# Optimization experiments

Measured on AMD Instinct MI355X. Metric: run time of the kernel, lower is better.

Reference implementation:

```python
import jax, jax.numpy as jnp
import numpy as np

N = 4096
IN_DIM, HID, OUT_DIM = 512, 256, 64
PROP_STEP = 10
LAM_HAT = 0.9
SCAD_A = 3.7
EPS = 1e-8


def setup_inputs() -> dict:
    key = jax.random.key(0)
    kA, kF, k1, k2 = jax.random.split(key, 4)
    # sparse symmetric 0/1 adjacency, zero diagonal (add_loops adds I later)
    u = jax.random.uniform(kA, (N, N), dtype=jnp.float32)
    A = (u < 0.005).astype(jnp.float32)
    A = jnp.maximum(A, A.T)
    A = A * (1.0 - jnp.eye(N, dtype=jnp.float32))
    F = jax.random.normal(kF, (N, IN_DIM), dtype=jnp.float32)
    W1 = jax.random.normal(k1, (IN_DIM, HID), dtype=jnp.float32) / np.sqrt(IN_DIM)
    b1 = jnp.zeros((HID,), dtype=jnp.float32)
    W2 = jax.random.normal(k2, (HID, OUT_DIM), dtype=jnp.float32) / np.sqrt(HID)
    b2 = jnp.zeros((OUT_DIM,), dtype=jnp.float32)
    raw_gamma = jnp.zeros((PROP_STEP,), dtype=jnp.float32)
    return {"A": A, "F": F, "W1": W1, "b1": b1, "W2": W2, "b2": b2,
            "raw_gamma": raw_gamma}


def reference(A, F, W1, b1, W2, b2, raw_gamma):
    lam = 1.0 / LAM_HAT - 1.0
    a = SCAD_A
    # MLP (dropout inactive at inference)
    F0 = jax.nn.relu(F @ W1 + b1) @ W2 + b2            # [N, out_dim]
    eye = jnp.eye(A.shape[0], dtype=A.dtype)
    A = A + eye                                        # add_loops
    D = A.sum(-1)                                      # [N]
    D_sq = jnp.sqrt(D)[:, None]                        # [N, 1]
    A_tilde = A / D_sq / D_sq.T                        # sym_norm: D^-1/2 A D^-1/2
    gammas = jax.nn.sigmoid(raw_gamma) * 2.0           # per-layer gamma in (0, 2)

    def step(Fc, gamma_k):
        Fn = Fc / D_sq
        nrm = jnp.linalg.norm(Fn, axis=-1, keepdims=True)
        Fu = Fn / jnp.maximum(nrm, 1e-12)
        # cosine distance in [0, 2]; detached as in torch (.detach())
        y = jax.lax.stop_gradient(1.0 - Fu @ Fu.T)     # [N, N]
        lam_k = jnp.maximum(gamma_k / a, EPS)
        t = a * lam_k
        safe_y = jnp.where(y <= 0.0, 1.0, y)
        w_mid = (t - y) / ((a - 1.0) * safe_y)
        # SCAD weight: 1 for y<=lam_k, linear decay on [lam_k, a*lam_k], 0 beyond
        W = jnp.where(y <= lam_k, 1.0, jnp.where(y <= t, w_mid, 0.0))
        W = W * (1.0 - eye)
        W = jnp.where(jnp.isnan(W), 1.0, W)
        Q_hat = ((W * A).sum(-1) / D + lam)[:, None]   # [N, 1]
        F_new = (W * A_tilde) @ Fc / Q_hat + lam * F0 / Q_hat
        return F_new, None

    F_out, _ = jax.lax.scan(step, F0, gammas)
    return F_out
```

## Files before the change

### kernel.cpp

```cpp
#include <hip/hip_runtime.h>
#include <hip/hip_bf16.h>

#define N_NODES 4096
#define IN_DIM  512
#define HID_DIM 256
#define OUT_DIM 64
#define PROP_STEP 10
#define MAX_DEG 128
#define GEMM_BLOCKS 512
#define SCAN_BLOCKS 512
#define LAM_CONST (1.0f/0.9f - 1.0f)
#define SCAD_A 3.7f

__device__ __forceinline__ ushort f2bf(float f) {
    unsigned u = __float_as_uint(f);
    unsigned r = (u + 0x7FFFu + ((u >> 16) & 1u)) >> 16;
    return (ushort)r;
}
__device__ __forceinline__ unsigned pack2(float lo, float hi) {
    return (unsigned)f2bf(lo) | ((unsigned)f2bf(hi) << 16);
}
__device__ __forceinline__ float bflo(unsigned u) { return __uint_as_float(u << 16); }
__device__ __forceinline__ float bfhi(unsigned u) { return __uint_as_float(u & 0xFFFF0000u); }
__device__ __forceinline__ float4 f4add(float4 a, float4 b) {
    return make_float4(a.x + b.x, a.y + b.y, a.z + b.z, a.w + b.w);
}

#define FMA32(A0, A1, WV) \
    ac0.x = fmaf(A0.x, WV.x, ac0.x); ac0.y = fmaf(A0.x, WV.y, ac0.y); \
    ac0.z = fmaf(A0.x, WV.z, ac0.z); ac0.w = fmaf(A0.x, WV.w, ac0.w); \
    ac1.x = fmaf(A0.y, WV.x, ac1.x); ac1.y = fmaf(A0.y, WV.y, ac1.y); \
    ac1.z = fmaf(A0.y, WV.z, ac1.z); ac1.w = fmaf(A0.y, WV.w, ac1.w); \
    ac2.x = fmaf(A0.z, WV.x, ac2.x); ac2.y = fmaf(A0.z, WV.y, ac2.y); \
    ac2.z = fmaf(A0.z, WV.z, ac2.z); ac2.w = fmaf(A0.z, WV.w, ac2.w); \
    ac3.x = fmaf(A0.w, WV.x, ac3.x); ac3.y = fmaf(A0.w, WV.y, ac3.y); \
    ac3.z = fmaf(A0.w, WV.z, ac3.z); ac3.w = fmaf(A0.w, WV.w, ac3.w); \
    ac4.x = fmaf(A1.x, WV.x, ac4.x); ac4.y = fmaf(A1.x, WV.y, ac4.y); \
    ac4.z = fmaf(A1.x, WV.z, ac4.z); ac4.w = fmaf(A1.x, WV.w, ac4.w); \
    ac5.x = fmaf(A1.y, WV.x, ac5.x); ac5.y = fmaf(A1.y, WV.y, ac5.y); \
    ac5.z = fmaf(A1.y, WV.z, ac5.z); ac5.w = fmaf(A1.y, WV.w, ac5.w); \
    ac6.x = fmaf(A1.z, WV.x, ac6.x); ac6.y = fmaf(A1.z, WV.y, ac6.y); \
    ac6.z = fmaf(A1.z, WV.z, ac6.z); ac6.w = fmaf(A1.z, WV.w, ac6.w); \
    ac7.x = fmaf(A1.w, WV.x, ac7.x); ac7.y = fmaf(A1.w, WV.y, ac7.y); \
    ac7.z = fmaf(A1.w, WV.z, ac7.z); ac7.w = fmaf(A1.w, WV.w, ac7.w);

#define CONS(KK, WV) { \
    float4 a0_ = *(const float4*)&sF[(KK) * 8];     \
    float4 a1_ = *(const float4*)&sF[(KK) * 8 + 4]; \
    FMA32(a0_, a1_, WV) }

#define P2ROW(HV, PV) \
    PV.x = fmaf(HV.x, w0.x, PV.x); PV.y = fmaf(HV.x, w0.y, PV.y); \
    PV.z = fmaf(HV.x, w0.z, PV.z); PV.w = fmaf(HV.x, w0.w, PV.w); \
    PV.x = fmaf(HV.y, w1.x, PV.x); PV.y = fmaf(HV.y, w1.y, PV.y); \
    PV.z = fmaf(HV.y, w1.z, PV.z); PV.w = fmaf(HV.y, w1.w, PV.w); \
    PV.x = fmaf(HV.z, w2.x, PV.x); PV.y = fmaf(HV.z, w2.y, PV.y); \
    PV.z = fmaf(HV.z, w2.z, PV.z); PV.w = fmaf(HV.z, w2.w, PV.w); \
    PV.x = fmaf(HV.w, w3.x, PV.x); PV.y = fmaf(HV.w, w3.y, PV.y); \
    PV.z = fmaf(HV.w, w3.z, PV.z); PV.w = fmaf(HV.w, w3.w, PV.w);

__global__ __launch_bounds__(256, 4) void build_all(
    const float* __restrict__ A, const float* __restrict__ F,
    const float* __restrict__ W1, const float* __restrict__ b1,
    const float* __restrict__ W2, const float* __restrict__ b2,
    float* __restrict__ F0,
    int* __restrict__ ell, int* __restrict__ deg,
    float* __restrict__ invD, float* __restrict__ invDsq)
{
    __shared__ float smem[8192];
    if (blockIdx.x >= SCAN_BLOCKS) {
        float* sF = smem;
        int t    = threadIdx.x;
        int lane = t & 63, wid = t >> 6;
        int m0   = (blockIdx.x - SCAN_BLOCKS) * 8;
        {
            int r = t & 7, kc = (t >> 3) * 16;
            const float* src = F + (size_t)(m0 + r) * IN_DIM + kc;
#pragma unroll
            for (int j = 0; j < 4; j++) {
                float4 v = *(const float4*)(src + j * 4);
                sF[(kc + j * 4 + 0) * 8 + r] = v.x;
                sF[(kc + j * 4 + 1) * 8 + r] = v.y;
                sF[(kc + j * 4 + 2) * 8 + r] = v.z;
                sF[(kc + j * 4 + 3) * 8 + r] = v.w;
            }
        }
        __syncthreads();
        int cg = lane;
        int kw = wid * 128;
        const float* Wp = W1 + (size_t)kw * HID_DIM + cg * 4;
        float4 ac0 = {0,0,0,0}, ac1 = {0,0,0,0}, ac2 = {0,0,0,0}, ac3 = {0,0,0,0};
        float4 ac4 = {0,0,0,0}, ac5 = {0,0,0,0}, ac6 = {0,0,0,0}, ac7 = {0,0,0,0};
        float4 wa0 = *(const float4*)(Wp + 0 * HID_DIM);
        float4 wa1 = *(const float4*)(Wp + 1 * HID_DIM);
        float4 wa2 = *(const float4*)(Wp + 2 * HID_DIM);
        float4 wa3 = *(const float4*)(Wp + 3 * HID_DIM);
        float4 wb0 = *(const float4*)(Wp + 4 * HID_DIM);
        float4 wb1 = *(const float4*)(Wp + 5 * HID_DIM);
        float4 wb2 = *(const float4*)(Wp + 6 * HID_DIM);
        float4 wb3 = *(const float4*)(Wp + 7 * HID_DIM);
        for (int kb = 0; kb < 128; kb += 8) {
            int k0 = kw + kb;
            CONS(k0 + 0, wa0) CONS(k0 + 1, wa1) CONS(k0 + 2, wa2) CONS(k0 + 3, wa3)
            if (kb + 8 < 128) {
                const float* wn = Wp + (size_t)(kb + 8) * HID_DIM;
                wa0 = *(const float4*)(wn);
                wa1 = *(const float4*)(wn + HID_DIM);
                wa2 = *(const float4*)(wn + 2 * HID_DIM);
                wa3 = *(const float4*)(wn + 3 * HID_DIM);
            }
            CONS(k0 + 4, wb0) CONS(k0 + 5, wb1) CONS(k0 + 6, wb2) CONS(k0 + 7, wb3)
            if (kb + 8 < 128) {
                const float* wn = Wp + (size_t)(kb + 12) * HID_DIM;
                wb0 = *(const float4*)(wn);
                wb1 = *(const float4*)(wn + HID_DIM);
                wb2 = *(const float4*)(wn + 2 * HID_DIM);
                wb3 = *(const float4*)(wn + 3 * HID_DIM);
            }
        }
        __syncthreads();
        {
            float* pp = smem + (size_t)wid * 2048;
            *(float4*)&pp[0 * 256 + cg * 4] = ac0;
            *(float4*)&pp[1 * 256 + cg * 4] = ac1;
            *(float4*)&pp[2 * 256 + cg * 4] = ac2;
            *(float4*)&pp[3 * 256 + cg * 4] = ac3;
            *(float4*)&pp[4 * 256 + cg * 4] = ac4;
            *(float4*)&pp[5 * 256 + cg * 4] = ac5;
            *(float4*)&pp[6 * 256 + cg * 4] = ac6;
            *(float4*)&pp[7 * 256 + cg * 4] = ac7;
        }
        __syncthreads();
        for (int i = t; i < 2048; i += 256) {
            float h = smem[i] + smem[i + 2048] + smem[i + 4096] + smem[i + 6144]
                    + b1[i & 255];
            smem[i] = fmaxf(h, 0.0f);
        }
        __syncthreads();
        float* sH = smem;
        int rgrp = lane >> 4;
        int cg2  = lane & 15;
        float4 p0 = {0,0,0,0}, p1 = {0,0,0,0};
        int kbase = wid * 64;
        for (int kq = 0; kq < 64; kq += 4) {
            int kg = kbase + kq;
            float4 h0 = *(const float4*)&sH[(rgrp * 2 + 0) * 256 + kg];
            float4 h1 = *(const float4*)&sH[(rgrp * 2 + 1) * 256 + kg];
            float4 w0 = *(const float4*)(W2 + (size_t)(kg + 0) * OUT_DIM + cg2 * 4);
            float4 w1 = *(const float4*)(W2 + (size_t)(kg + 1) * OUT_DIM + cg2 * 4);
            float4 w2 = *(const float4*)(W2 + (size_t)(kg + 2) * OUT_DIM + cg2 * 4);
            float4 w3 = *(const float4*)(W2 + (size_t)(kg + 3) * OUT_DIM + cg2 * 4);
            P2ROW(h0, p0) P2ROW(h1, p1)
        }
        __syncthreads();
        if (wid) {
            float* dst = smem + 2048 + (size_t)(wid - 1) * 512 + lane * 8;
            *(float4*)(dst + 0) = p0;
            *(float4*)(dst + 4) = p1;
        }
        __syncthreads();
        if (wid == 0) {
#pragma unroll
            for (int w = 0; w < 3; w++) {
                const float* s = smem + 2048 + (size_t)w * 512 + lane * 8;
                p0 = f4add(p0, *(const float4*)(s + 0));
                p1 = f4add(p1, *(const float4*)(s + 4));
            }
            float4 b2v = *(const float4*)(b2 + cg2 * 4);
            float* o = F0 + (size_t)(m0 + rgrp * 2) * OUT_DIM + cg2 * 4;
            *(float4*)(o + 0 * OUT_DIM) = f4add(p0, b2v);
            *(float4*)(o + 1 * OUT_DIM) = f4add(p1, b2v);
        }
    } else {
        int sb   = blockIdx.x;
        int lane = threadIdx.x & 63;
        int wid  = threadIdx.x >> 6;
        int w    = sb * 4 + wid;
        for (int rr = 0; rr < 2; rr++) {
            int row = w * 2 + rr;
            const float* Arow = A + (size_t)row * N_NODES;
            float4 ch[16];
#pragma unroll
            for (int c = 0; c < 16; c++)
                ch[c] = *(const float4*)(Arow + c * 256 + lane * 4);
            int* rdst = ell + (size_t)row * MAX_DEG;
            unsigned cnt = 0;
#pragma unroll
            for (int c = 0; c < 16; c++) {
                float4 v = ch[c];
                int colbase = c * 256 + lane * 4;
#pragma unroll
                for (int q = 0; q < 4; q++) {
                    float vv = (q == 0) ? v.x : (q == 1) ? v.y : (q == 2) ? v.z : v.w;
                    bool nz = (vv != 0.0f);
                    unsigned long long m = __ballot(nz);
                    unsigned rank = __builtin_amdgcn_mbcnt_hi(
                        (unsigned)(m >> 32),
                        __builtin_amdgcn_mbcnt_lo((unsigned)m, 0u));
                    unsigned pos = cnt + rank;
                    if (nz && pos < MAX_DEG) rdst[pos] = colbase + q;
                    cnt += (unsigned)__popcll(m);
                }
            }
            int c  = (cnt > MAX_DEG) ? MAX_DEG : (int)cnt;
            int pad = (c + 15) & ~15;
            if (pad > MAX_DEG) pad = MAX_DEG;
            if (lane >= c && lane < pad) rdst[lane] = row;
            int l2 = lane + 64;
            if (l2 >= c && l2 < pad) rdst[l2] = row;
            if (lane == 0) {
                deg[row] = c;
                float d = (float)(cnt + 1);
                invD[row] = 1.0f / d;
                invDsq[row] = rsqrtf(d);
            }
        }
    }
}

__global__ __launch_bounds__(256, 4) void propagate_f0(
    const float* __restrict__ F0,
    const int* __restrict__ ell, const int* __restrict__ deg,
    const float* __restrict__ invD, const float* __restrict__ invDsq,
    const float* __restrict__ raw_gamma,
    unsigned* __restrict__ Pout, float* __restrict__ nrmOut)
{
    int lane = threadIdx.x & 63;
    int wid  = threadIdx.x >> 6;
    int r    = __builtin_amdgcn_readfirstlane(blockIdx.x * 4 + wid);
    int g    = lane >> 3;
    int sl   = lane & 7;
    const float inv_am1 = 1.0f / (SCAD_A - 1.0f);

    float gamma = 2.0f / (1.0f + expf(-raw_gamma[0]));
    float lam_k = fmaxf(gamma / SCAD_A, 1e-8f);
    float tt    = SCAD_A * lam_k;

    int dg = deg[r];
    int pad = (dg + 15) & ~15;
    int npair = pad >> 4;
    const int* nb = ell + (size_t)r * MAX_DEG;
    int ed0 = (lane < pad)      ? nb[lane]      : r;
    int ed1 = (64 + lane < pad) ? nb[64 + lane] : r;

    float iDs = invDsq[r];
    const float4* f04 = (const float4*)(F0 + (size_t)r * OUT_DIM + sl * 8);
    float4 fa = f04[0], fb = f04[1];
    float f0v[8] = { fa.x, fa.y, fa.z, fa.w, fb.x, fb.y, fb.z, fb.w };
    float ui[8];
    float ssr = 0.0f;
#pragma unroll
    for (int q = 0; q < 8; q++) { ui[q] = f0v[q] * iDs; ssr += ui[q] * ui[q]; }
    ssr += __shfl_xor(ssr, 1, 64);
    ssr += __shfl_xor(ssr, 2, 64);
    ssr += __shfl_xor(ssr, 4, 64);
    float inv_nr = 1.0f / fmaxf(sqrtf(ssr), 1e-12f);
#pragma unroll
    for (int q = 0; q < 8; q++) ui[q] *= inv_nr;

    float acc[8] = {};
    float qsum = 0.0f;
    for (int it = 0; it < npair; ++it) {
        int e0 = it * 16 + g, e1 = e0 + 8;
        int src = (it < 4) ? ed0 : ed1;
        int j0 = __shfl(src, e0 & 63, 64);
        int j1 = __shfl(src, e1 & 63, 64);
        const float4* p0 = (const float4*)(F0 + (size_t)j0 * OUT_DIM + sl * 8);
        const float4* p1 = (const float4*)(F0 + (size_t)j1 * OUT_DIM + sl * 8);
        float4 x0 = p0[0], x1 = p0[1];
        float4 y0 = p1[0], y1 = p1[1];
        float d0 = invDsq[j0], d1 = invDsq[j1];
        float v0[8] = { x0.x*d0, x0.y*d0, x0.z*d0, x0.w*d0, x1.x*d0, x1.y*d0, x1.z*d0, x1.w*d0 };
        float v1[8] = { y0.x*d1, y0.y*d1, y0.z*d1, y0.w*d1, y1.x*d1, y1.y*d1, y1.z*d1, y1.w*d1 };
        float pa = 0.f, pb = 0.f, s0 = 0.f, s1 = 0.f;
#pragma unroll
        for (int q = 0; q < 8; q++) {
            pa += ui[q] * v0[q]; s0 += v0[q] * v0[q];
            pb += ui[q] * v1[q]; s1 += v1[q] * v1[q];
        }
        pa += __shfl_xor(pa, 1, 64); pb += __shfl_xor(pb, 1, 64);
        s0 += __shfl_xor(s0, 1, 64); s1 += __shfl_xor(s1, 1, 64);
        pa += __shfl_xor(pa, 2, 64); pb += __shfl_xor(pb, 2, 64);
        s0 += __shfl_xor(s0, 2, 64); s1 += __shfl_xor(s1, 2, 64);
        pa += __shfl_xor(pa, 4, 64); pb += __shfl_xor(pb, 4, 64);
        s0 += __shfl_xor(s0, 4, 64); s1 += __shfl_xor(s1, 4, 64);
        float n0 = fmaxf(sqrtf(s0), 1e-12f);
        float n1 = fmaxf(sqrtf(s1), 1e-12f);
        float ya = 1.0f - pa / n0, yb = 1.0f - pb / n1;
        float wa = (ya <= lam_k) ? 1.0f : ((ya <= tt) ? (tt - ya) * inv_am1 / ya : 0.0f);
        float wb = (yb <= lam_k) ? 1.0f : ((yb <= tt) ? (tt - yb) * inv_am1 / yb : 0.0f);
        if (e0 >= dg) wa = 0.0f;
        if (e1 >= dg) wb = 0.0f;
        qsum += wa + wb;
#pragma unroll
        for (int q = 0; q < 8; q++) acc[q] += wa * v0[q] + wb * v1[q];
    }

#pragma unroll
    for (int off = 8; off <= 32; off <<= 1) {
#pragma unroll
        for (int q = 0; q < 8; q++) acc[q] += __shfl_xor(acc[q], off, 64);
        qsum += __shfl_xor(qsum, off, 64);
    }

    float Qh  = qsum * invD[r] + LAM_CONST;
    float rQh = 1.0f / Qh;
    float res[8], fn[8];
    float ssq = 0.0f;
#pragma unroll
    for (int q = 0; q < 8; q++) {
        res[q] = (acc[q] * iDs + LAM_CONST * f0v[q]) * rQh;
        fn[q]  = res[q] * iDs;
        ssq   += fn[q] * fn[q];
    }
    ssq += __shfl_xor(ssq, 1, 64);
    ssq += __shfl_xor(ssq, 2, 64);
    ssq += __shfl_xor(ssq, 4, 64);
    float nrm = fmaxf(sqrtf(ssq), 1e-12f);
    float inv_n = 1.0f / nrm;
    if (lane < 8) {
        uint4 fuPk;
        fuPk.x = pack2(fn[0] * inv_n, fn[1] * inv_n);
        fuPk.y = pack2(fn[2] * inv_n, fn[3] * inv_n);
        fuPk.z = pack2(fn[4] * inv_n, fn[5] * inv_n);
        fuPk.w = pack2(fn[6] * inv_n, fn[7] * inv_n);
        *(uint4*)(Pout + (size_t)r * 32 + sl * 4) = fuPk;
    }
    if (lane == 0) nrmOut[r] = nrm;
}

__global__ __launch_bounds__(256, 4) void propagate(
    const unsigned* __restrict__ Pin, const float* __restrict__ nrmIn,
    const float* __restrict__ F0,
    const int* __restrict__ ell, const int* __restrict__ deg,
    const float* __restrict__ invD, const float* __restrict__ invDsq,
    const float* __restrict__ raw_gamma, int step,
    unsigned* __restrict__ Pout, float* __restrict__ nrmOut,
    float* __restrict__ FcOut, int writeNext, int writeOut)
{
    int lane = threadIdx.x & 63;
    int wid  = threadIdx.x >> 6;
    int r    = __builtin_amdgcn_readfirstlane(blockIdx.x * 4 + wid);
    int g    = lane >> 3;
    int sl   = lane & 7;
    const float inv_am1 = 1.0f / (SCAD_A - 1.0f);

    float gamma = 2.0f / (1.0f + expf(-raw_gamma[step]));
    float lam_k = fmaxf(gamma / SCAD_A, 1e-8f);
    float tt    = SCAD_A * lam_k;

    int dg = deg[r];
    int pad = (dg + 15) & ~15;
    int npair = pad >> 4;
    const int* nb = ell + (size_t)r * MAX_DEG;
    int ed0 = (lane < pad)      ? nb[lane]      : r;
    int ed1 = (64 + lane < pad) ? nb[64 + lane] : r;

    uint4 up = *(const uint4*)(Pin + (size_t)r * 32 + sl * 4);
    float ui[8] = { bflo(up.x), bfhi(up.x), bflo(up.y), bfhi(up.y),
                    bflo(up.z), bfhi(up.z), bflo(up.w), bfhi(up.w) };

    float acc[8] = {};
    float qsum = 0.0f;

    auto eidx = [&](int it_, int& J0, int& J1) {
        int e0_ = it_ * 16 + g;
        int src = (it_ < 4) ? ed0 : ed1;
        J0 = __shfl(src, e0_ & 63, 64);
        J1 = __shfl(src, (e0_ + 8) & 63, 64);
    };
    auto body = [&](int it_, uint4 U0, uint4 U1, float NR0, float NR1) {
        float pa = ui[0] * bflo(U0.x) + ui[1] * bfhi(U0.x) + ui[2] * bflo(U0.y) + ui[3] * bfhi(U0.y)
                 + ui[4] * bflo(U0.z) + ui[5] * bfhi(U0.z) + ui[6] * bflo(U0.w) + ui[7] * bfhi(U0.w);
        float pb = ui[0] * bflo(U1.x) + ui[1] * bfhi(U1.x) + ui[2] * bflo(U1.y) + ui[3] * bfhi(U1.y)
                 + ui[4] * bflo(U1.z) + ui[5] * bfhi(U1.z) + ui[6] * bflo(U1.w) + ui[7] * bfhi(U1.w);
        pa += __shfl_xor(pa, 1, 64); pb += __shfl_xor(pb, 1, 64);
        pa += __shfl_xor(pa, 2, 64); pb += __shfl_xor(pb, 2, 64);
        pa += __shfl_xor(pa, 4, 64); pb += __shfl_xor(pb, 4, 64);
        float ya = 1.0f - pa, yb = 1.0f - pb;
        float wa = (ya <= lam_k) ? 1.0f : ((ya <= tt) ? (tt - ya) * inv_am1 / ya : 0.0f);
        float wb = (yb <= lam_k) ? 1.0f : ((yb <= tt) ? (tt - yb) * inv_am1 / yb : 0.0f);
        int e0_ = it_ * 16 + g;
        if (e0_ >= dg)     wa = 0.0f;
        if (e0_ + 8 >= dg) wb = 0.0f;
        qsum += wa + wb;
        float wsa = wa * NR0;
        float wsb = wb * NR1;
        acc[0] += wsa * bflo(U0.x) + wsb * bflo(U1.x);
        acc[1] += wsa * bfhi(U0.x) + wsb * bfhi(U1.x);
        acc[2] += wsa * bflo(U0.y) + wsb * bflo(U1.y);
        acc[3] += wsa * bfhi(U0.y) + wsb * bfhi(U1.y);
        acc[4] += wsa * bflo(U0.z) + wsb * bflo(U1.z);
        acc[5] += wsa * bfhi(U0.z) + wsb * bfhi(U1.z);
        acc[6] += wsa * bflo(U0.w) + wsb * bflo(U1.w);
        acc[7] += wsa * bfhi(U0.w) + wsb * bfhi(U1.w);
    };

    if (npair > 0) {
        uint4 uA0, uA1, uB0, uB1;
        float nA0, nA1, nB0, nB1;
        int j0, j1;
        eidx(0, j0, j1);
        uA0 = *(const uint4*)(Pin + (size_t)j0 * 32 + sl * 4);
        uA1 = *(const uint4*)(Pin + (size_t)j1 * 32 + sl * 4);
        nA0 = nrmIn[j0]; nA1 = nrmIn[j1];
        int it = 0;
        while (true) {
            if (it + 1 < npair) {
                eidx(it + 1, j0, j1);
                uB0 = *(const uint4*)(Pin + (size_t)j0 * 32 + sl * 4);
                uB1 = *(const uint4*)(Pin + (size_t)j1 * 32 + sl * 4);
                nB0 = nrmIn[j0]; nB1 = nrmIn[j1];
            }
            body(it, uA0, uA1, nA0, nA1);
            ++it; if (it >= npair) break;
            if (it + 1 < npair) {
                eidx(it + 1, j0, j1);
                uA0 = *(const uint4*)(Pin + (size_t)j0 * 32 + sl * 4);
                uA1 = *(const uint4*)(Pin + (size_t)j1 * 32 + sl * 4);
                nA0 = nrmIn[j0]; nA1 = nrmIn[j1];
            }
            body(it, uB0, uB1, nB0, nB1);
            ++it; if (it >= npair) break;
        }
    }

#pragma unroll
    for (int off = 8; off <= 32; off <<= 1) {
#pragma unroll
        for (int q = 0; q < 8; q++) acc[q] += __shfl_xor(acc[q], off, 64);
        qsum += __shfl_xor(qsum, off, 64);
    }

    float iDs = invDsq[r];
    float Qh  = qsum * invD[r] + LAM_CONST;
    float rQh = 1.0f / Qh;
    const float4* f04 = (const float4*)(F0 + (size_t)r * OUT_DIM + sl * 8);
    float4 f0a = f04[0], f0b = f04[1];
    float f0v[8] = { f0a.x, f0a.y, f0a.z, f0a.w, f0b.x, f0b.y, f0b.z, f0b.w };
    float res[8];
#pragma unroll
    for (int q = 0; q < 8; q++) res[q] = (acc[q] * iDs + LAM_CONST * f0v[q]) * rQh;

    if (writeOut && lane < 8) {
        float4* o4 = (float4*)(FcOut + (size_t)r * OUT_DIM + sl * 8);
        o4[0] = make_float4(res[0], res[1], res[2], res[3]);
        o4[1] = make_float4(res[4], res[5], res[6], res[7]);
    }
    if (writeNext) {
        float fn[8];
        float ssq = 0.0f;
#pragma unroll
        for (int q = 0; q < 8; q++) { fn[q] = res[q] * iDs; ssq += fn[q] * fn[q]; }
        ssq += __shfl_xor(ssq, 1, 64);
        ssq += __shfl_xor(ssq, 2, 64);
        ssq += __shfl_xor(ssq, 4, 64);
        float nrm = fmaxf(sqrtf(ssq), 1e-12f);
        float inv_n = 1.0f / nrm;
        if (lane < 8) {
            uint4 fuPk;
            fuPk.x = pack2(fn[0] * inv_n, fn[1] * inv_n);
            fuPk.y = pack2(fn[2] * inv_n, fn[3] * inv_n);
            fuPk.z = pack2(fn[4] * inv_n, fn[5] * inv_n);
            fuPk.w = pack2(fn[6] * inv_n, fn[7] * inv_n);
            *(uint4*)(Pout + (size_t)r * 32 + sl * 4) = fuPk;
        }
        if (lane == 0) nrmOut[r] = nrm;
    }
}

extern "C" void kernel_launch(void* const* d_in, const int* in_sizes, int n_in,
                              void* d_out, int out_size, void* d_ws, size_t ws_size,
                              hipStream_t stream)
{
    const float* A  = (const float*)d_in[0];
    const float* F  = (const float*)d_in[1];
    const float* W1 = (const float*)d_in[2];
    const float* b1 = (const float*)d_in[3];
    const float* W2 = (const float*)d_in[4];
    const float* b2 = (const float*)d_in[5];
    const float* rg = (const float*)d_in[6];
    float* out = (float*)d_out;

    char* p = (char*)d_ws;
    float* F0     = (float*)p; p += (size_t)N_NODES * OUT_DIM * 4;
    unsigned* Pa  = (unsigned*)p; p += (size_t)N_NODES * 32 * 4;
    unsigned* Pb  = (unsigned*)p; p += (size_t)N_NODES * 32 * 4;
    float* nrmA   = (float*)p; p += (size_t)N_NODES * 4;
    float* nrmB   = (float*)p; p += (size_t)N_NODES * 4;
    float* invD   = (float*)p; p += (size_t)N_NODES * 4;
    float* invDsq = (float*)p; p += (size_t)N_NODES * 4;
    int*   deg    = (int*)p;   p += (size_t)N_NODES * 4;
    int*   ell    = (int*)p;   p += (size_t)N_NODES * MAX_DEG * 4;

    build_all<<<GEMM_BLOCKS + SCAN_BLOCKS, 256, 0, stream>>>(
        A, F, W1, b1, W2, b2, F0, ell, deg, invD, invDsq);

    propagate_f0<<<N_NODES / 4, 256, 0, stream>>>(
        F0, ell, deg, invD, invDsq, rg, Pa, nrmA);

    for (int k = 1; k < PROP_STEP; k++) {
        unsigned* Pin   = (k & 1) ? Pa : Pb;
        unsigned* Pout  = (k & 1) ? Pb : Pa;
        float* nIn      = (k & 1) ? nrmA : nrmB;
        float* nOut     = (k & 1) ? nrmB : nrmA;
        int last = (k == PROP_STEP - 1);
        propagate<<<N_NODES / 4, 256, 0, stream>>>(
            Pin, nIn, F0, ell, deg, invD, invDsq, rg, k,
            Pout, nOut, out, !last, last);
    }
}
```

Measured before the change: 195.5 us.

## Fuse all propagation steps into one persistent kernel with per-node flag sync

Replaces the ten separate propagate launches with a single kernel. Each wavefront owns one node and iterates all layers. Per-layer packed features and norms go to distinct buffers, and the nonzero norm value serves as a ready flag that neighbours spin on with agent-scope atomic loads. This removes the launch and grid-wide barrier cost between steps, but it depends on all 1024 blocks being co-resident to avoid deadlock, and it drops the software prefetch pipelining that the old loop had.

```diff
diff --git a/kernel.cpp b/kernel.cpp
--- a/kernel.cpp
+++ b/kernel.cpp
@@ -11,6 +11,7 @@
 #define SCAN_BLOCKS 512
 #define LAM_CONST (1.0f/0.9f - 1.0f)
 #define SCAD_A 3.7f
+#define PSTRIDE_U ((size_t)N_NODES * 32)
 
 __device__ __forceinline__ ushort f2bf(float f) {
     unsigned u = __float_as_uint(f);
@@ -65,7 +66,8 @@
     const float* __restrict__ W2, const float* __restrict__ b2,
     float* __restrict__ F0,
     int* __restrict__ ell, int* __restrict__ deg,
-    float* __restrict__ invD, float* __restrict__ invDsq)
+    float* __restrict__ invD, float* __restrict__ invDsq,
+    float* __restrict__ nrmZ)
 {
     __shared__ float smem[8192];
     if (blockIdx.x >= SCAN_BLOCKS) {
@@ -172,6 +174,9 @@
             *(float4*)(o + 1 * OUT_DIM) = f4add(p1, b2v);
         }
     } else {
+        for (int i = (int)blockIdx.x * 256 + threadIdx.x;
+             i < (PROP_STEP - 1) * N_NODES; i += SCAN_BLOCKS * 256)
+            nrmZ[i] = 0.0f;
         int sb   = blockIdx.x;
         int lane = threadIdx.x & 63;
         int wid  = threadIdx.x >> 6;
@@ -218,238 +223,101 @@
     }
 }
 
-__global__ __launch_bounds__(256, 4) void propagate_f0(
+__global__ __launch_bounds__(256, 4) void propagate_all(
     const float* __restrict__ F0,
     const int* __restrict__ ell, const int* __restrict__ deg,
     const float* __restrict__ invD, const float* __restrict__ invDsq,
     const float* __restrict__ raw_gamma,
-    unsigned* __restrict__ Pout, float* __restrict__ nrmOut)
+    unsigned* __restrict__ Pl, float* __restrict__ nrmL,
+    float* __restrict__ out)
 {
     int lane = threadIdx.x & 63;
     int wid  = threadIdx.x >> 6;
-    int r    = __builtin_amdgcn_readfirstlane(blockIdx.x * 4 + wid);
+    int r    = __builtin_amdgcn_readfirstlane((int)blockIdx.x * 4 + wid);
     int g    = lane >> 3;
     int sl   = lane & 7;
     const float inv_am1 = 1.0f / (SCAD_A - 1.0f);
 
-    float gamma = 2.0f / (1.0f + expf(-raw_gamma[0]));
-    float lam_k = fmaxf(gamma / SCAD_A, 1e-8f);
-    float tt    = SCAD_A * lam_k;
-
-    int dg = deg[r];
+    int dg  = deg[r];
     int pad = (dg + 15) & ~15;
     int npair = pad >> 4;
     const int* nb = ell + (size_t)r * MAX_DEG;
     int ed0 = (lane < pad)      ? nb[lane]      : r;
     int ed1 = (64 + lane < pad) ? nb[64 + lane] : r;
-
     float iDs = invDsq[r];
+    float iD  = invD[r];
     const float4* f04 = (const float4*)(F0 + (size_t)r * OUT_DIM + sl * 8);
     float4 fa = f04[0], fb = f04[1];
     float f0v[8] = { fa.x, fa.y, fa.z, fa.w, fb.x, fb.y, fb.z, fb.w };
+
     float ui[8];
-    float ssr = 0.0f;
-#pragma unroll
-    for (int q = 0; q < 8; q++) { ui[q] = f0v[q] * iDs; ssr += ui[q] * ui[q]; }
-    ssr += __shfl_xor(ssr, 1, 64);
-    ssr += __shfl_xor(ssr, 2, 64);
-    ssr += __shfl_xor(ssr, 4, 64);
-    float inv_nr = 1.0f / fmaxf(sqrtf(ssr), 1e-12f);
-#pragma unroll
-    for (int q = 0; q < 8; q++) ui[q] *= inv_nr;
-
-    float acc[8] = {};
-    float qsum = 0.0f;
-    for (int it = 0; it < npair; ++it) {
-        int e0 = it * 16 + g, e1 = e0 + 8;
-        int src = (it < 4) ? ed0 : ed1;
-        int j0 = __shfl(src, e0 & 63, 64);
-        int j1 = __shfl(src, e1 & 63, 64);
-        const float4* p0 = (const float4*)(F0 + (size_t)j0 * OUT_DIM + sl * 8);
-        const float4* p1 = (const float4*)(F0 + (size_t)j1 * OUT_DIM + sl * 8);
-        float4 x0 = p0[0], x1 = p0[1];
-        float4 y0 = p1[0], y1 = p1[1];
-        float d0 = invDsq[j0], d1 = invDsq[j1];
-        float v0[8] = { x0.x*d0, x0.y*d0, x0.z*d0, x0.w*d0, x1.x*d0, x1.y*d0, x1.z*d0, x1.w*d0 };
-        float v1[8] = { y0.x*d1, y0.y*d1, y0.z*d1, y0.w*d1, y1.x*d1, y1.y*d1, y1.z*d1, y1.w*d1 };
-        float pa = 0.f, pb = 0.f, s0 = 0.f, s1 = 0.f;
-#pragma unroll
-        for (int q = 0; q < 8; q++) {
-            pa += ui[q] * v0[q]; s0 += v0[q] * v0[q];
-            pb += ui[q] * v1[q]; s1 += v1[q] * v1[q];
-        }
-        pa += __shfl_xor(pa, 1, 64); pb += __shfl_xor(pb, 1, 64);
-        s0 += __shfl_xor(s0, 1, 64); s1 += __shfl_xor(s1, 1, 64);
-        pa += __shfl_xor(pa, 2, 64); pb += __shfl_xor(pb, 2, 64);
-        s0 += __shfl_xor(s0, 2, 64); s1 += __shfl_xor(s1, 2, 64);
-        pa += __shfl_xor(pa, 4, 64); pb += __shfl_xor(pb, 4, 64);
-        s0 += __shfl_xor(s0, 4, 64); s1 += __shfl_xor(s1, 4, 64);
-        float n0 = fmaxf(sqrtf(s0), 1e-12f);
-        float n1 = fmaxf(sqrtf(s1), 1e-12f);
-        float ya = 1.0f - pa / n0, yb = 1.0f - pb / n1;
-        float wa = (ya <= lam_k) ? 1.0f : ((ya <= tt) ? (tt - ya) * inv_am1 / ya : 0.0f);
-        float wb = (yb <= lam_k) ? 1.0f : ((yb <= tt) ? (tt - yb) * inv_am1 / yb : 0.0f);
-        if (e0 >= dg) wa = 0.0f;
-        if (e1 >= dg) wb = 0.0f;
-        qsum += wa + wb;
-#pragma unroll
-        for (int q = 0; q < 8; q++) acc[q] += wa * v0[q] + wb * v1[q];
+    float res[8];
+
+    {
+        float gamma = 2.0f / (1.0f + expf(-raw_gamma[0]));
+        float lam_k = fmaxf(gamma / SCAD_A, 1e-8f);
+        float tt    = SCAD_A * lam_k;
+        float ssr = 0.0f;
+#pragma unroll
+        for (int q = 0; q < 8; q++) { ui[q] = f0v[q] * iDs; ssr += ui[q] * ui[q]; }
+        ssr += __shfl_xor(ssr, 1, 64);
+        ssr += __shfl_xor(ssr, 2, 64);
+        ssr += __shfl_xor(ssr, 4, 64);
+        float inv_nr = 1.0f / fmaxf(sqrtf(ssr), 1e-12f);
+#pragma unroll
+        for (int q = 0; q < 8; q++) ui[q] *= inv_nr;
+
+        float acc[8] = {};
+        float qsum = 0.0f;
+        for (int it = 0; it < npair; ++it) {
+            int e0 = it * 16 + g, e1 = e0 + 8;
+            int src = (it < 4) ? ed0 : ed1;
+            int j0 = __shfl(src, e0 & 63, 64);
+            int j1 = __shfl(src, e1 & 63, 64);
+            const float4* p0 = (const float4*)(F0 + (size_t)j0 * OUT_DIM + sl * 8);
+            const float4* p1 = (const float4*)(F0 + (size_t)j1 * OUT_DIM + sl * 8);
+            float4 x0 = p0[0], x1 = p0[1];
+            float4 y0 = p1[0], y1 = p1[1];
+            float d0 = invDsq[j0], d1 = invDsq[j1];
+            float v0[8] = { x0.x*d0, x0.y*d0, x0.z*d0, x0.w*d0, x1.x*d0, x1.y*d0, x1.z*d0, x1.w*d0 };
+            float v1[8] = { y0.x*d1, y0.y*d1, y0.z*d1, y0.w*d1, y1.x*d1, y1.y*d1, y1.z*d1, y1.w*d1 };
+            float pa = 0.f, pb = 0.f, s0 = 0.f, s1 = 0.f;
+#pragma unroll
+            for (int q = 0; q < 8; q++) {
+                pa += ui[q] * v0[q]; s0 += v0[q] * v0[q];
+                pb += ui[q] * v1[q]; s1 += v1[q] * v1[q];
+            }
+            pa += __shfl_xor(pa, 1, 64); pb += __shfl_xor(pb, 1, 64);
+            s0 += __shfl_xor(s0, 1, 64); s1 += __shfl_xor(s1, 1, 64);
+            pa += __shfl_xor(pa, 2, 64); pb += __shfl_xor(pb, 2, 64);
+            s0 += __shfl_xor(s0, 2, 64); s1 += __shfl_xor(s1, 2, 64);
+            pa += __shfl_xor(pa, 4, 64); pb += __shfl_xor(pb, 4, 64);
+            s0 += __shfl_xor(s0, 4, 64); s1 += __shfl_xor(s1, 4, 64);
+            float n0 = fmaxf(sqrtf(s0), 1e-12f);
+            float n1 = fmaxf(sqrtf(s1), 1e-12f);
+            float ya = 1.0f - pa / n0, yb = 1.0f - pb / n1;
+            float wa = (ya <= lam_k) ? 1.0f : ((ya <= tt) ? (tt - ya) * inv_am1 / ya : 0.0f);
+            float wb = (yb <= lam_k) ? 1.0f : ((yb <= tt) ? (tt - yb) * inv_am1 / yb : 0.0f);
+            if (e0 >= dg) wa = 0.0f;
+            if (e1 >= dg) wb = 0.0f;
+            qsum += wa + wb;
+#pragma unroll
+            for (int q = 0; q < 8; q++) acc[q] += wa * v0[q] + wb * v1[q];
+        }
+#pragma unroll
+        for (int off = 8; off <= 32; off <<= 1) {
+#pragma unroll
+            for (int q = 0; q < 8; q++) acc[q] += __shfl_xor(acc[q], off, 64);
+            qsum += __shfl_xor(qsum, off, 64);
+        }
+        float Qh  = qsum * iD + LAM_CONST;
+        float rQh = 1.0f / Qh;
+#pragma unroll
+        for (int q = 0; q < 8; q++) res[q] = (acc[q] * iDs + LAM_CONST * f0v[q]) * rQh;
     }
 
-#pragma unroll
-    for (int off = 8; off <= 32; off <<= 1) {
-#pragma unroll
-        for (int q = 0; q < 8; q++) acc[q] += __shfl_xor(acc[q], off, 64);
-        qsum += __shfl_xor(qsum, off, 64);
-    }
-
-    float Qh  = qsum * invD[r] + LAM_CONST;
-    float rQh = 1.0f / Qh;
-    float res[8], fn[8];
-    float ssq = 0.0f;
-#pragma unroll
-    for (int q = 0; q < 8; q++) {
-        res[q] = (acc[q] * iDs + LAM_CONST * f0v[q]) * rQh;
-        fn[q]  = res[q] * iDs;
-        ssq   += fn[q] * fn[q];
-    }
-    ssq += __shfl_xor(ssq, 1, 64);
-    ssq += __shfl_xor(ssq, 2, 64);
-    ssq += __shfl_xor(ssq, 4, 64);
-    float nrm = fmaxf(sqrtf(ssq), 1e-12f);
-    float inv_n = 1.0f / nrm;
-    if (lane < 8) {
-        uint4 fuPk;
-        fuPk.x = pack2(fn[0] * inv_n, fn[1] * inv_n);
-        fuPk.y = pack2(fn[2] * inv_n, fn[3] * inv_n);
-        fuPk.z = pack2(fn[4] * inv_n, fn[5] * inv_n);
-        fuPk.w = pack2(fn[6] * inv_n, fn[7] * inv_n);
-        *(uint4*)(Pout + (size_t)r * 32 + sl * 4) = fuPk;
-    }
-    if (lane == 0) nrmOut[r] = nrm;
-}
-
-__global__ __launch_bounds__(256, 4) void propagate(
-    const unsigned* __restrict__ Pin, const float* __restrict__ nrmIn,
-    const float* __restrict__ F0,
-    const int* __restrict__ ell, const int* __restrict__ deg,
-    const float* __restrict__ invD, const float* __restrict__ invDsq,
-    const float* __restrict__ raw_gamma, int step,
-    unsigned* __restrict__ Pout, float* __restrict__ nrmOut,
-    float* __restrict__ FcOut, int writeNext, int writeOut)
-{
-    int lane = threadIdx.x & 63;
-    int wid  = threadIdx.x >> 6;
-    int r    = __builtin_amdgcn_readfirstlane(blockIdx.x * 4 + wid);
-    int g    = lane >> 3;
-    int sl   = lane & 7;
-    const float inv_am1 = 1.0f / (SCAD_A - 1.0f);
-
-    float gamma = 2.0f / (1.0f + expf(-raw_gamma[step]));
-    float lam_k = fmaxf(gamma / SCAD_A, 1e-8f);
-    float tt    = SCAD_A * lam_k;
-
-    int dg = deg[r];
-    int pad = (dg + 15) & ~15;
-    int npair = pad >> 4;
-    const int* nb = ell + (size_t)r * MAX_DEG;
-    int ed0 = (lane < pad)      ? nb[lane]      : r;
-    int ed1 = (64 + lane < pad) ? nb[64 + lane] : r;
-
-    uint4 up = *(const uint4*)(Pin + (size_t)r * 32 + sl * 4);
-    float ui[8] = { bflo(up.x), bfhi(up.x), bflo(up.y), bfhi(up.y),
-                    bflo(up.z), bfhi(up.z), bflo(up.w), bfhi(up.w) };
-
-    float acc[8] = {};
-    float qsum = 0.0f;
-
-    auto eidx = [&](int it_, int& J0, int& J1) {
-        int e0_ = it_ * 16 + g;
-        int src = (it_ < 4) ? ed0 : ed1;
-        J0 = __shfl(src, e0_ & 63, 64);
-        J1 = __shfl(src, (e0_ + 8) & 63, 64);
-    };
-    auto body = [&](int it_, uint4 U0, uint4 U1, float NR0, float NR1) {
-        float pa = ui[0] * bflo(U0.x) + ui[1] * bfhi(U0.x) + ui[2] * bflo(U0.y) + ui[3] * bfhi(U0.y)
-                 + ui[4] * bflo(U0.z) + ui[5] * bfhi(U0.z) + ui[6] * bflo(U0.w) + ui[7] * bfhi(U0.w);
-        float pb = ui[0] * bflo(U1.x) + ui[1] * bfhi(U1.x) + ui[2] * bflo(U1.y) + ui[3] * bfhi(U1.y)
-                 + ui[4] * bflo(U1.z) + ui[5] * bfhi(U1.z) + ui[6] * bflo(U1.w) + ui[7] * bfhi(U1.w);
-        pa += __shfl_xor(pa, 1, 64); pb += __shfl_xor(pb, 1, 64);
-        pa += __shfl_xor(pa, 2, 64); pb += __shfl_xor(pb, 2, 64);
-        pa += __shfl_xor(pa, 4, 64); pb += __shfl_xor(pb, 4, 64);
-        float ya = 1.0f - pa, yb = 1.0f - pb;
-        float wa = (ya <= lam_k) ? 1.0f : ((ya <= tt) ? (tt - ya) * inv_am1 / ya : 0.0f);
-        float wb = (yb <= lam_k) ? 1.0f : ((yb <= tt) ? (tt - yb) * inv_am1 / yb : 0.0f);
-        int e0_ = it_ * 16 + g;
-        if (e0_ >= dg)     wa = 0.0f;
-        if (e0_ + 8 >= dg) wb = 0.0f;
-        qsum += wa + wb;
-        float wsa = wa * NR0;
-        float wsb = wb * NR1;
-        acc[0] += wsa * bflo(U0.x) + wsb * bflo(U1.x);
-        acc[1] += wsa * bfhi(U0.x) + wsb * bfhi(U1.x);
-        acc[2] += wsa * bflo(U0.y) + wsb * bflo(U1.y);
-        acc[3] += wsa * bfhi(U0.y) + wsb * bfhi(U1.y);
-        acc[4] += wsa * bflo(U0.z) + wsb * bflo(U1.z);
-        acc[5] += wsa * bfhi(U0.z) + wsb * bfhi(U1.z);
-        acc[6] += wsa * bflo(U0.w) + wsb * bflo(U1.w);
-        acc[7] += wsa * bfhi(U0.w) + wsb * bfhi(U1.w);
-    };
-
-    if (npair > 0) {
-        uint4 uA0, uA1, uB0, uB1;
-        float nA0, nA1, nB0, nB1;
-        int j0, j1;
-        eidx(0, j0, j1);
-        uA0 = *(const uint4*)(Pin + (size_t)j0 * 32 + sl * 4);
-        uA1 = *(const uint4*)(Pin + (size_t)j1 * 32 + sl * 4);
-        nA0 = nrmIn[j0]; nA1 = nrmIn[j1];
-        int it = 0;
-        while (true) {
-            if (it + 1 < npair) {
-                eidx(it + 1, j0, j1);
-                uB0 = *(const uint4*)(Pin + (size_t)j0 * 32 + sl * 4);
-                uB1 = *(const uint4*)(Pin + (size_t)j1 * 32 + sl * 4);
-                nB0 = nrmIn[j0]; nB1 = nrmIn[j1];
-            }
-            body(it, uA0, uA1, nA0, nA1);
-            ++it; if (it >= npair) break;
-            if (it + 1 < npair) {
-                eidx(it + 1, j0, j1);
-                uA0 = *(const uint4*)(Pin + (size_t)j0 * 32 + sl * 4);
-                uA1 = *(const uint4*)(Pin + (size_t)j1 * 32 + sl * 4);
-                nA0 = nrmIn[j0]; nA1 = nrmIn[j1];
-            }
-            body(it, uB0, uB1, nB0, nB1);
-            ++it; if (it >= npair) break;
-        }
-    }
-
-#pragma unroll
-    for (int off = 8; off <= 32; off <<= 1) {
-#pragma unroll
-        for (int q = 0; q < 8; q++) acc[q] += __shfl_xor(acc[q], off, 64);
-        qsum += __shfl_xor(qsum, off, 64);
-    }
-
-    float iDs = invDsq[r];
-    float Qh  = qsum * invD[r] + LAM_CONST;
-    float rQh = 1.0f / Qh;
-    const float4* f04 = (const float4*)(F0 + (size_t)r * OUT_DIM + sl * 8);
-    float4 f0a = f04[0], f0b = f04[1];
-    float f0v[8] = { f0a.x, f0a.y, f0a.z, f0a.w, f0b.x, f0b.y, f0b.z, f0b.w };
-    float res[8];
-#pragma unroll
-    for (int q = 0; q < 8; q++) res[q] = (acc[q] * iDs + LAM_CONST * f0v[q]) * rQh;
-
-    if (writeOut && lane < 8) {
-        float4* o4 = (float4*)(FcOut + (size_t)r * OUT_DIM + sl * 8);
-        o4[0] = make_float4(res[0], res[1], res[2], res[3]);
-        o4[1] = make_float4(res[4], res[5], res[6], res[7]);
-    }
-    if (writeNext) {
-        float fn[8];
-        float ssq = 0.0f;
+    for (int l = 1; l < PROP_STEP; ++l) {
+        float fn[8]; float ssq = 0.0f;
 #pragma unroll
         for (int q = 0; q < 8; q++) { fn[q] = res[q] * iDs; ssq += fn[q] * fn[q]; }
         ssq += __shfl_xor(ssq, 1, 64);
@@ -457,15 +325,102 @@
         ssq += __shfl_xor(ssq, 4, 64);
         float nrm = fmaxf(sqrtf(ssq), 1e-12f);
         float inv_n = 1.0f / nrm;
+        uint4 fuPk;
+        fuPk.x = pack2(fn[0] * inv_n, fn[1] * inv_n);
+        fuPk.y = pack2(fn[2] * inv_n, fn[3] * inv_n);
+        fuPk.z = pack2(fn[4] * inv_n, fn[5] * inv_n);
+        fuPk.w = pack2(fn[6] * inv_n, fn[7] * inv_n);
+        unsigned* Pc = Pl + (size_t)(l - 1) * PSTRIDE_U;
+        float*    nc = nrmL + (size_t)(l - 1) * N_NODES;
         if (lane < 8) {
-            uint4 fuPk;
-            fuPk.x = pack2(fn[0] * inv_n, fn[1] * inv_n);
-            fuPk.y = pack2(fn[2] * inv_n, fn[3] * inv_n);
-            fuPk.z = pack2(fn[4] * inv_n, fn[5] * inv_n);
-            fuPk.w = pack2(fn[6] * inv_n, fn[7] * inv_n);
-            *(uint4*)(Pout + (size_t)r * 32 + sl * 4) = fuPk;
-        }
-        if (lane == 0) nrmOut[r] = nrm;
+            unsigned long long q0 = (unsigned long long)fuPk.x | ((unsigned long long)fuPk.y << 32);
+            unsigned long long q1 = (unsigned long long)fuPk.z | ((unsigned long long)fuPk.w << 32);
+            unsigned long long* dst = (unsigned long long*)(Pc + (size_t)r * 32 + sl * 4);
+            __hip_atomic_store(dst,     q0, __ATOMIC_RELAXED, __HIP_MEMORY_SCOPE_AGENT);
+            __hip_atomic_store(dst + 1, q1, __ATOMIC_RELAXED, __HIP_MEMORY_SCOPE_AGENT);
+        }
+        asm volatile("s_waitcnt vmcnt(0)" ::: "memory");
+        if (lane == 0)
+            __hip_atomic_store((int*)(nc + r), __float_as_int(nrm),
+                               __ATOMIC_RELAXED, __HIP_MEMORY_SCOPE_AGENT);
+        ui[0] = bflo(fuPk.x); ui[1] = bfhi(fuPk.x);
+        ui[2] = bflo(fuPk.y); ui[3] = bfhi(fuPk.y);
+        ui[4] = bflo(fuPk.z); ui[5] = bfhi(fuPk.z);
+        ui[6] = bflo(fuPk.w); ui[7] = bfhi(fuPk.w);
+
+        float gamma = 2.0f / (1.0f + expf(-raw_gamma[l]));
+        float lam_k = fmaxf(gamma / SCAD_A, 1e-8f);
+        float tt    = SCAD_A * lam_k;
+
+        float acc[8] = {};
+        float qsum = 0.0f;
+        for (int it = 0; it < npair; ++it) {
+            int e0 = it * 16 + g, e1 = e0 + 8;
+            int src = (it < 4) ? ed0 : ed1;
+            int j0 = __shfl(src, e0 & 63, 64);
+            int j1 = __shfl(src, e1 & 63, 64);
+            int* fp0 = (int*)(nc + j0);
+            int* fp1 = (int*)(nc + j1);
+            int b0 = __hip_atomic_load(fp0, __ATOMIC_RELAXED, __HIP_MEMORY_SCOPE_AGENT);
+            int b1 = __hip_atomic_load(fp1, __ATOMIC_RELAXED, __HIP_MEMORY_SCOPE_AGENT);
+            while (!__all((b0 != 0) && (b1 != 0))) {
+                __builtin_amdgcn_s_sleep(8);
+                b0 = __hip_atomic_load(fp0, __ATOMIC_RELAXED, __HIP_MEMORY_SCOPE_AGENT);
+                b1 = __hip_atomic_load(fp1, __ATOMIC_RELAXED, __HIP_MEMORY_SCOPE_AGENT);
+            }
+            float nr0 = __uint_as_float((unsigned)b0);
+            float nr1 = __uint_as_float((unsigned)b1);
+            asm volatile("" ::: "memory");
+            unsigned long long* g0 = (unsigned long long*)(Pc + (size_t)j0 * 32 + sl * 4);
+            unsigned long long* g1 = (unsigned long long*)(Pc + (size_t)j1 * 32 + sl * 4);
+            unsigned long long d00 = __hip_atomic_load(g0,     __ATOMIC_RELAXED, __HIP_MEMORY_SCOPE_AGENT);
+            unsigned long long d01 = __hip_atomic_load(g0 + 1, __ATOMIC_RELAXED, __HIP_MEMORY_SCOPE_AGENT);
+            unsigned long long d10 = __hip_atomic_load(g1,     __ATOMIC_RELAXED, __HIP_MEMORY_SCOPE_AGENT);
+            unsigned long long d11 = __hip_atomic_load(g1 + 1, __ATOMIC_RELAXED, __HIP_MEMORY_SCOPE_AGENT);
+            uint4 U0 = make_uint4((unsigned)d00, (unsigned)(d00 >> 32),
+                                  (unsigned)d01, (unsigned)(d01 >> 32));
+            uint4 U1 = make_uint4((unsigned)d10, (unsigned)(d10 >> 32),
+                                  (unsigned)d11, (unsigned)(d11 >> 32));
+            float pa = ui[0] * bflo(U0.x) + ui[1] * bfhi(U0.x) + ui[2] * bflo(U0.y) + ui[3] * bfhi(U0.y)
+                     + ui[4] * bflo(U0.z) + ui[5] * bfhi(U0.z) + ui[6] * bflo(U0.w) + ui[7] * bfhi(U0.w);
+            float pb = ui[0] * bflo(U1.x) + ui[1] * bfhi(U1.x) + ui[2] * bflo(U1.y) + ui[3] * bfhi(U1.y)
+                     + ui[4] * bflo(U1.z) + ui[5] * bfhi(U1.z) + ui[6] * bflo(U1.w) + ui[7] * bfhi(U1.w);
+            pa += __shfl_xor(pa, 1, 64); pb += __shfl_xor(pb, 1, 64);
+            pa += __shfl_xor(pa, 2, 64); pb += __shfl_xor(pb, 2, 64);
+            pa += __shfl_xor(pa, 4, 64); pb += __shfl_xor(pb, 4, 64);
+            float ya = 1.0f - pa, yb = 1.0f - pb;
+            float wa = (ya <= lam_k) ? 1.0f : ((ya <= tt) ? (tt - ya) * inv_am1 / ya : 0.0f);
+            float wb = (yb <= lam_k) ? 1.0f : ((yb <= tt) ? (tt - yb) * inv_am1 / yb : 0.0f);
+            if (e0 >= dg) wa = 0.0f;
+            if (e1 >= dg) wb = 0.0f;
+            qsum += wa + wb;
+            float wsa = wa * nr0;
+            float wsb = wb * nr1;
+            acc[0] += wsa * bflo(U0.x) + wsb * bflo(U1.x);
+            acc[1] += wsa * bfhi(U0.x) + wsb * bfhi(U1.x);
+            acc[2] += wsa * bflo(U0.y) + wsb * bflo(U1.y);
+            acc[3] += wsa * bfhi(U0.y) + wsb * bfhi(U1.y);
+            acc[4] += wsa * bflo(U0.z) + wsb * bflo(U1.z);
+            acc[5] += wsa * bfhi(U0.z) + wsb * bfhi(U1.z);
+            acc[6] += wsa * bflo(U0.w) + wsb * bflo(U1.w);
+            acc[7] += wsa * bfhi(U0.w) + wsb * bfhi(U1.w);
+        }
+#pragma unroll
+        for (int off = 8; off <= 32; off <<= 1) {
+#pragma unroll
+            for (int q = 0; q < 8; q++) acc[q] += __shfl_xor(acc[q], off, 64);
+            qsum += __shfl_xor(qsum, off, 64);
+        }
+        float Qh  = qsum * iD + LAM_CONST;
+        float rQh = 1.0f / Qh;
+#pragma unroll
+        for (int q = 0; q < 8; q++) res[q] = (acc[q] * iDs + LAM_CONST * f0v[q]) * rQh;
+    }
+
+    if (lane < 8) {
+        float4* o4 = (float4*)(out + (size_t)r * OUT_DIM + sl * 8);
+        o4[0] = make_float4(res[0], res[1], res[2], res[3]);
+        o4[1] = make_float4(res[4], res[5], res[6], res[7]);
     }
 }
 
@@ -484,29 +439,16 @@
 
     char* p = (char*)d_ws;
     float* F0     = (float*)p; p += (size_t)N_NODES * OUT_DIM * 4;
-    unsigned* Pa  = (unsigned*)p; p += (size_t)N_NODES * 32 * 4;
-    unsigned* Pb  = (unsigned*)p; p += (size_t)N_NODES * 32 * 4;
-    float* nrmA   = (float*)p; p += (size_t)N_NODES * 4;
-    float* nrmB   = (float*)p; p += (size_t)N_NODES * 4;
+    unsigned* Pl  = (unsigned*)p; p += (size_t)(PROP_STEP - 1) * PSTRIDE_U * 4;
+    float* nrmL   = (float*)p; p += (size_t)(PROP_STEP - 1) * N_NODES * 4;
     float* invD   = (float*)p; p += (size_t)N_NODES * 4;
     float* invDsq = (float*)p; p += (size_t)N_NODES * 4;
     int*   deg    = (int*)p;   p += (size_t)N_NODES * 4;
     int*   ell    = (int*)p;   p += (size_t)N_NODES * MAX_DEG * 4;
 
     build_all<<<GEMM_BLOCKS + SCAN_BLOCKS, 256, 0, stream>>>(
-        A, F, W1, b1, W2, b2, F0, ell, deg, invD, invDsq);
-
-    propagate_f0<<<N_NODES / 4, 256, 0, stream>>>(
-        F0, ell, deg, invD, invDsq, rg, Pa, nrmA);
-
-    for (int k = 1; k < PROP_STEP; k++) {
-        unsigned* Pin   = (k & 1) ? Pa : Pb;
-        unsigned* Pout  = (k & 1) ? Pb : Pa;
-        float* nIn      = (k & 1) ? nrmA : nrmB;
-        float* nOut     = (k & 1) ? nrmB : nrmA;
-        int last = (k == PROP_STEP - 1);
-        propagate<<<N_NODES / 4, 256, 0, stream>>>(
-            Pin, nIn, F0, ell, deg, invD, invDsq, rg, k,
-            Pout, nOut, out, !last, last);
-    }
-}
+        A, F, W1, b1, W2, b2, F0, ell, deg, invD, invDsq, nrmL);
+
+    propagate_all<<<N_NODES / 4, 256, 0, stream>>>(
+        F0, ell, deg, invD, invDsq, rg, Pl, nrmL, out);
+}
```

Result: slower. 272.3 us (+39.3%).
